# Kernel tuning notes

Measured on AMD Instinct MI355X. Metric: run time of the kernel, lower is better.

The kernel has to match this reference:

```python
import jax, jax.numpy as jnp
import numpy as np

DIM = 1024
HEADS = 16
HEAD_DIM = DIM // HEADS
SCALE = DIM ** -0.5  # note: original uses full dim, not head_dim


def setup_inputs() -> dict:
    key = jax.random.key(0)
    k1, k2, k3, k4 = jax.random.split(key, 4)
    x = jax.random.normal(k1, (4, 2048, DIM), dtype=jnp.float32)
    # nn.Linear(dim, 3*dim, bias=False): weight [3*dim, dim]; y = x @ W.T
    w_qkv = jax.random.normal(k2, (3 * DIM, DIM), dtype=jnp.float32) * (DIM ** -0.5)
    w_out = jax.random.normal(k3, (DIM, DIM), dtype=jnp.float32) * (DIM ** -0.5)
    b_out = jax.random.normal(k4, (DIM,), dtype=jnp.float32) * 0.01
    return {"x": x, "w_qkv": w_qkv, "w_out": w_out, "b_out": b_out}


def reference(x, w_qkv, w_out, b_out):
    b, n, d = x.shape
    qkv = jnp.einsum('bnd,ed->bne', x, w_qkv)  # [b, n, 3*dim]
    # rearrange 'b n (qkv h d) -> qkv b h n d'
    qkv = qkv.reshape(b, n, 3, HEADS, HEAD_DIM).transpose(2, 0, 3, 1, 4)
    q, k, v = qkv[0], qkv[1], qkv[2]
    dots = jnp.einsum('bhid,bhjd->bhij', q, k) * SCALE
    attn = jax.nn.softmax(dots, axis=-1)
    out = jnp.einsum('bhij,bhjd->bhid', attn, v)
    out = out.transpose(0, 2, 1, 3).reshape(b, n, d)  # b h n d -> b n (h d)
    return jnp.einsum('bnd,ed->bne', out, w_out) + b_out
```

## Files before the change

kernel.cpp:

```cpp
#include <hip/hip_runtime.h>
#include <stdint.h>
#include <stddef.h>

typedef _Float16 f16;
typedef __attribute__((ext_vector_type(8))) _Float16 f16x8;
typedef __attribute__((ext_vector_type(4))) _Float16 f16x4;
typedef __attribute__((ext_vector_type(4))) float f32x4;

#define DINL __device__ __forceinline__

DINL void async_cp16(void* lds, const void* gmem) {
    __builtin_amdgcn_global_load_lds(
        (const __attribute__((address_space(1))) void*)(uintptr_t)gmem,
        (__attribute__((address_space(3))) void*)(uint32_t)(uintptr_t)lds,
        16, 0, 0);
}

__global__ void cast_f32_f16(const float* __restrict__ src, f16* __restrict__ dst,
                             int n4, int scale_n4, float scale) {
    int stride = gridDim.x * blockDim.x;
    for (int i = blockIdx.x * blockDim.x + threadIdx.x; i < n4; i += stride) {
        float4 v = ((const float4*)src)[i];
        float s = (i < scale_n4) ? scale : 1.f;
        f16x4 h = { (f16)(v.x * s), (f16)(v.y * s), (f16)(v.z * s), (f16)(v.w * s) };
        ((f16x4*)dst)[i] = h;
    }
}

template <typename TC, bool HAS_BIAS>
__global__ __launch_bounds__(256) void gemm_bt(
    const f16* __restrict__ A, const f16* __restrict__ B,
    TC* __restrict__ C, const float* __restrict__ bias,
    int M, int N, int K)
{
    constexpr int BK = 64;
    __shared__ __align__(16) f16 As[128 * BK];
    __shared__ __align__(16) f16 Bs[128 * BK];

    const int tid  = threadIdx.x;
    const int lane = tid & 63;
    const int wave = tid >> 6;
    const int bm = blockIdx.y * 128;
    const int bn = blockIdx.x * 128;
    const int wr = (wave >> 1) * 64;
    const int wc = (wave & 1) * 64;

    f32x4 acc[4][4] = {};

    for (int k0 = 0; k0 < K; k0 += BK) {
#pragma unroll
        for (int it = 0; it < 4; ++it) {
            int s = tid + it * 256, row = s >> 3, cc = (s & 7) ^ (row & 7);
            async_cp16(&As[(size_t)s * 8], &A[(size_t)(bm + row) * K + k0 + cc * 8]);
        }
#pragma unroll
        for (int it = 0; it < 4; ++it) {
            int s = tid + it * 256, row = s >> 3, cc = (s & 7) ^ (row & 7);
            async_cp16(&Bs[(size_t)s * 8], &B[(size_t)(bn + row) * K + k0 + cc * 8]);
        }
        __syncthreads();

#pragma unroll
        for (int ks = 0; ks < BK; ks += 32) {
            const int rlo = lane & 15;
            const int c = (ks >> 3) + (lane >> 4);
            f16x8 af[4], bf[4];
#pragma unroll
            for (int m = 0; m < 4; ++m) {
                int r = wr + m * 16 + rlo;
                af[m] = *(const f16x8*)&As[(r * 8 + (c ^ (r & 7))) * 8];
            }
#pragma unroll
            for (int n = 0; n < 4; ++n) {
                int r = wc + n * 16 + rlo;
                bf[n] = *(const f16x8*)&Bs[(r * 8 + (c ^ (r & 7))) * 8];
            }
#pragma unroll
            for (int m = 0; m < 4; ++m)
#pragma unroll
                for (int n = 0; n < 4; ++n)
                    acc[m][n] = __builtin_amdgcn_mfma_f32_16x16x32_f16(af[m], bf[n], acc[m][n], 0, 0, 0);
        }
        __syncthreads();
    }

#pragma unroll
    for (int n = 0; n < 4; ++n) {
        const int gc = bn + wc + n * 16 + (lane & 15);
        float bv = 0.f;
        if constexpr (HAS_BIAS) bv = bias[gc];
#pragma unroll
        for (int m = 0; m < 4; ++m) {
            const int gr0 = bm + wr + m * 16 + ((lane >> 4) << 2);
#pragma unroll
            for (int r = 0; r < 4; ++r) {
                float v = acc[m][n][r] + bv;
                if constexpr (sizeof(TC) == 4) C[(size_t)(gr0 + r) * N + gc] = v;
                else                           C[(size_t)(gr0 + r) * N + gc] = (f16)v;
            }
        }
    }
}

__global__ __launch_bounds__(256) void transpose_v(const f16* __restrict__ qkv, f16* __restrict__ vt) {
    __shared__ float T[64][65];
    const int bid = blockIdx.x, bh = bid >> 5, st = bid & 31;
    const int b = bh >> 4, h = bh & 15, s0 = st * 64;
    const int tid = threadIdx.x;
    const int rs = tid >> 2, c0 = (tid & 3) * 16;
    const f16* src = &qkv[(size_t)(b * 2048 + s0 + rs) * 3072 + 2048 + h * 64 + c0];
    f16x8 v0 = ((const f16x8*)src)[0], v1 = ((const f16x8*)src)[1];
#pragma unroll
    for (int e = 0; e < 8; ++e) { T[rs][c0 + e] = (float)v0[e]; T[rs][c0 + 8 + e] = (float)v1[e]; }
    __syncthreads();
    const int rd = tid >> 2, k0 = (tid & 3) * 16;
    f16x8 w0, w1;
#pragma unroll
    for (int e = 0; e < 8; ++e) { w0[e] = (f16)T[k0 + e][rd]; w1[e] = (f16)T[k0 + 8 + e][rd]; }
    f16* dst = &vt[(size_t)(bh * 64 + rd) * 2048 + s0 + k0];
    ((f16x8*)dst)[0] = w0; ((f16x8*)dst)[1] = w1;
}

__global__ __launch_bounds__(256) void attn_mfma(
    const f16* __restrict__ qkv, const f16* __restrict__ vt, f16* __restrict__ out)
{
    constexpr int TD = 3072;
    __shared__ __align__(16) f16 Qs[128 * 64];
    __shared__ __align__(16) f16 Ks[64 * 64];
    __shared__ __align__(16) f16 Vs[64 * 64];
    __shared__ __align__(16) f16 Ps[4][32 * 64];

    const int tid = threadIdx.x, lane = tid & 63, wave = tid >> 6;
    const int bh = blockIdx.x, b = bh >> 4, h = bh & 15;
    const int q0 = blockIdx.y * 128;
    const size_t base = (size_t)b * 2048 * TD + h * 64;
    const int lo = lane & 15, hi = lane >> 4;

#pragma unroll
    for (int it = 0; it < 4; ++it) {
        int s = tid + it * 256, row = s >> 3, cc = (s & 7) ^ (row & 7);
        async_cp16(&Qs[s * 8], &qkv[base + (size_t)(q0 + row) * TD + cc * 8]);
    }

    float lp[2][4] = {};
    f32x4 o_[2][4] = {};

    for (int jt = 0; jt < 32; ++jt) {
        {
            int s = tid, row = s >> 3, cc = (s & 7) ^ (row & 7);
            int s2 = tid + 256, row2 = s2 >> 3, cc2 = (s2 & 7) ^ (row2 & 7);
            async_cp16(&Ks[s * 8],  &qkv[base + 1024 + (size_t)(jt * 64 + row)  * TD + cc * 8]);
            async_cp16(&Ks[s2 * 8], &qkv[base + 1024 + (size_t)(jt * 64 + row2) * TD + cc2 * 8]);
            async_cp16(&Vs[s * 8],  &vt[(size_t)(bh * 64 + row)  * 2048 + jt * 64 + cc * 8]);
            async_cp16(&Vs[s2 * 8], &vt[(size_t)(bh * 64 + row2) * 2048 + jt * 64 + cc2 * 8]);
        }
        __syncthreads();

        f32x4 sc[2][4] = {};
#pragma unroll
        for (int ks = 0; ks < 2; ++ks) {
            int c = ks * 4 + hi;
            f16x8 af[2];
#pragma unroll
            for (int m = 0; m < 2; ++m) {
                int r = wave * 32 + m * 16 + lo;
                af[m] = *(const f16x8*)&Qs[(r * 8 + (c ^ (r & 7))) * 8];
            }
#pragma unroll
            for (int n = 0; n < 4; ++n) {
                int key = n * 16 + lo;
                f16x8 bf = *(const f16x8*)&Ks[(key * 8 + (c ^ (key & 7))) * 8];
#pragma unroll
                for (int m = 0; m < 2; ++m)
                    sc[m][n] = __builtin_amdgcn_mfma_f32_16x16x32_f16(af[m], bf, sc[m][n], 0, 0, 0);
            }
        }

#pragma unroll
        for (int m = 0; m < 2; ++m) {
#pragma unroll
            for (int r = 0; r < 4; ++r) {
                float p0 = exp2f(sc[m][0][r]), p1 = exp2f(sc[m][1][r]);
                float p2 = exp2f(sc[m][2][r]), p3 = exp2f(sc[m][3][r]);
                lp[m][r] += (p0 + p1) + (p2 + p3);
                const int row_w = m * 16 + hi * 4 + r;
                const int rw7 = row_w & 7;
                const int ebase = row_w * 64 + (lo & 7);
                float pv[4] = { p0, p1, p2, p3 };
#pragma unroll
                for (int n = 0; n < 4; ++n) {
                    int chunk = n * 2 + (lo >> 3);
                    Ps[wave][ebase + ((chunk ^ rw7) << 3)] = (f16)pv[n];
                }
            }
        }
        asm volatile("s_waitcnt lgkmcnt(0)" ::: "memory");

#pragma unroll
        for (int ks = 0; ks < 2; ++ks) {
            int c = ks * 4 + hi;
            f16x8 pa[2];
#pragma unroll
            for (int m = 0; m < 2; ++m) {
                int r = m * 16 + lo;
                pa[m] = *(const f16x8*)&Ps[wave][(r * 8 + (c ^ (r & 7))) * 8];
            }
#pragma unroll
            for (int n = 0; n < 4; ++n) {
                int dd = n * 16 + lo;
                f16x8 vb = *(const f16x8*)&Vs[(dd * 8 + (c ^ (dd & 7))) * 8];
#pragma unroll
                for (int m = 0; m < 2; ++m)
                    o_[m][n] = __builtin_amdgcn_mfma_f32_16x16x32_f16(pa[m], vb, o_[m][n], 0, 0, 0);
            }
        }
        __syncthreads();
    }

#pragma unroll
    for (int m = 0; m < 2; ++m)
#pragma unroll
        for (int r = 0; r < 4; ++r) {
#pragma unroll
            for (int off = 1; off < 16; off <<= 1)
                lp[m][r] += __shfl_xor(lp[m][r], off);
            float inv = 1.f / lp[m][r];
            int row = q0 + wave * 32 + m * 16 + hi * 4 + r;
#pragma unroll
            for (int n = 0; n < 4; ++n) {
                int dim = h * 64 + n * 16 + lo;
                out[(size_t)(b * 2048 + row) * 1024 + dim] = (f16)(o_[m][n][r] * inv);
            }
        }
}

extern "C" void kernel_launch(void* const* d_in, const int* in_sizes, int n_in,
                              void* d_out, int out_size, void* d_ws, size_t ws_size,
                              hipStream_t stream)
{
    int ix = 0, iq = 1, iw = 2, ib = 3;
    for (int i = 0; i < n_in; ++i) {
        if      (in_sizes[i] == 8388608) ix = i;
        else if (in_sizes[i] == 3145728) iq = i;
        else if (in_sizes[i] == 1048576) iw = i;
        else if (in_sizes[i] == 1024)    ib = i;
    }
    const float* x     = (const float*)d_in[ix];
    const float* w_qkv = (const float*)d_in[iq];
    const float* w_out = (const float*)d_in[iw];
    const float* b_out = (const float*)d_in[ib];

    char* ws = (char*)d_ws;
    f16* Xh    = (f16*)(ws + 0);
    f16* AOh   = Xh;
    f16* Wqkvh = (f16*)(ws + 16777216);
    f16* Wouth = Wqkvh;
    f16* QKVh  = (f16*)(ws + 23068672);
    f16* Vth   = (f16*)(ws + 73400320);

    const float QSCALE = 0.03125f * 1.4426950408889634f;

    cast_f32_f16<<<2048, 256, 0, stream>>>(x,     Xh,    2097152, 0, 1.f);
    cast_f32_f16<<<1024, 256, 0, stream>>>(w_qkv, Wqkvh, 786432, 262144, QSCALE);

    gemm_bt<f16, false><<<dim3(24, 64), 256, 0, stream>>>(
        Xh, Wqkvh, QKVh, nullptr, 8192, 3072, 1024);

    cast_f32_f16<<<512, 256, 0, stream>>>(w_out, Wouth, 262144, 0, 1.f);

    transpose_v<<<2048, 256, 0, stream>>>(QKVh, Vth);

    attn_mfma<<<dim3(64, 16), 256, 0, stream>>>(QKVh, Vth, AOh);

    gemm_bt<float, true><<<dim3(8, 64), 256, 0, stream>>>(
        AOh, Wouth, (float*)d_out, b_out, 8192, 1024, 1024);
}
```

Before: 345.8 us.

## Double-buffer K/V tiles in attention, halve query tile, fuse cast kernels

The attention kernel now double-buffers K and V in LDS, prefetching the next tile while computing the current one, and drops one barrier per iteration. The query tile shrinks from 128 to 64 rows, so the grid doubles to 2048 blocks and each wave handles 16 rows instead of 32, which lowers register pressure and raises occupancy. The three f32-to-f16 cast launches are merged into one kernel, and w_out gets its own workspace slot so it no longer has to be cast after the QKV GEMM. In exchange, K/V are reloaded by twice as many blocks, and each K/V fragment read from LDS feeds half as many MFMAs.

```diff
diff --git a/kernel.cpp b/kernel.cpp
--- a/kernel.cpp
+++ b/kernel.cpp
@@ -16,14 +16,20 @@
         16, 0, 0);
 }
 
-__global__ void cast_f32_f16(const float* __restrict__ src, f16* __restrict__ dst,
-                             int n4, int scale_n4, float scale) {
+__global__ void cast_fused(const float* __restrict__ x, f16* __restrict__ xh,
+                           const float* __restrict__ wq, f16* __restrict__ wqh,
+                           const float* __restrict__ wo, f16* __restrict__ woh,
+                           float qs) {
     int stride = gridDim.x * blockDim.x;
-    for (int i = blockIdx.x * blockDim.x + threadIdx.x; i < n4; i += stride) {
-        float4 v = ((const float4*)src)[i];
-        float s = (i < scale_n4) ? scale : 1.f;
+    for (int i = blockIdx.x * blockDim.x + threadIdx.x; i < 3145728; i += stride) {
+        const float4* src; f16x4* dst; float s = 1.f;
+        if (i < 2097152)      { src = (const float4*)x  + i;            dst = (f16x4*)xh  + i; }
+        else if (i < 2883584) { int j = i - 2097152; src = (const float4*)wq + j; dst = (f16x4*)wqh + j;
+                                if (j < 262144) s = qs; }
+        else                  { int j = i - 2883584; src = (const float4*)wo + j; dst = (f16x4*)woh + j; }
+        float4 v = *src;
         f16x4 h = { (f16)(v.x * s), (f16)(v.y * s), (f16)(v.z * s), (f16)(v.w * s) };
-        ((f16x4*)dst)[i] = h;
+        *dst = h;
     }
 }
 
@@ -121,117 +127,105 @@
     ((f16x8*)dst)[0] = w0; ((f16x8*)dst)[1] = w1;
 }
 
+DINL void stage_kv(f16* Kd, f16* Vd, const f16* qkv, const f16* vt,
+                   size_t base, int bh, int jt, int tid) {
+    int s = tid, row = s >> 3, cc = (s & 7) ^ (row & 7);
+    int s2 = tid + 256, row2 = s2 >> 3, cc2 = (s2 & 7) ^ (row2 & 7);
+    async_cp16(&Kd[s * 8],  &qkv[base + 1024 + (size_t)(jt * 64 + row)  * 3072 + cc * 8]);
+    async_cp16(&Kd[s2 * 8], &qkv[base + 1024 + (size_t)(jt * 64 + row2) * 3072 + cc2 * 8]);
+    async_cp16(&Vd[s * 8],  &vt[(size_t)(bh * 64 + row)  * 2048 + jt * 64 + cc * 8]);
+    async_cp16(&Vd[s2 * 8], &vt[(size_t)(bh * 64 + row2) * 2048 + jt * 64 + cc2 * 8]);
+}
+
 __global__ __launch_bounds__(256) void attn_mfma(
     const f16* __restrict__ qkv, const f16* __restrict__ vt, f16* __restrict__ out)
 {
     constexpr int TD = 3072;
-    __shared__ __align__(16) f16 Qs[128 * 64];
-    __shared__ __align__(16) f16 Ks[64 * 64];
-    __shared__ __align__(16) f16 Vs[64 * 64];
-    __shared__ __align__(16) f16 Ps[4][32 * 64];
+    __shared__ __align__(16) f16 Qs[64 * 64];
+    __shared__ __align__(16) f16 Ks[2][64 * 64];
+    __shared__ __align__(16) f16 Vs[2][64 * 64];
+    __shared__ __align__(16) f16 Ps[4][16 * 64];
 
     const int tid = threadIdx.x, lane = tid & 63, wave = tid >> 6;
     const int bh = blockIdx.x, b = bh >> 4, h = bh & 15;
-    const int q0 = blockIdx.y * 128;
+    const int q0 = blockIdx.y * 64;
     const size_t base = (size_t)b * 2048 * TD + h * 64;
     const int lo = lane & 15, hi = lane >> 4;
 
 #pragma unroll
-    for (int it = 0; it < 4; ++it) {
+    for (int it = 0; it < 2; ++it) {
         int s = tid + it * 256, row = s >> 3, cc = (s & 7) ^ (row & 7);
         async_cp16(&Qs[s * 8], &qkv[base + (size_t)(q0 + row) * TD + cc * 8]);
     }
-
-    float lp[2][4] = {};
-    f32x4 o_[2][4] = {};
+    stage_kv(Ks[0], Vs[0], qkv, vt, base, bh, 0, tid);
+
+    float lp[4] = {};
+    f32x4 o_[4] = {};
 
     for (int jt = 0; jt < 32; ++jt) {
-        {
-            int s = tid, row = s >> 3, cc = (s & 7) ^ (row & 7);
-            int s2 = tid + 256, row2 = s2 >> 3, cc2 = (s2 & 7) ^ (row2 & 7);
-            async_cp16(&Ks[s * 8],  &qkv[base + 1024 + (size_t)(jt * 64 + row)  * TD + cc * 8]);
-            async_cp16(&Ks[s2 * 8], &qkv[base + 1024 + (size_t)(jt * 64 + row2) * TD + cc2 * 8]);
-            async_cp16(&Vs[s * 8],  &vt[(size_t)(bh * 64 + row)  * 2048 + jt * 64 + cc * 8]);
-            async_cp16(&Vs[s2 * 8], &vt[(size_t)(bh * 64 + row2) * 2048 + jt * 64 + cc2 * 8]);
-        }
+        const int cur = jt & 1;
         __syncthreads();
-
-        f32x4 sc[2][4] = {};
+        if (jt + 1 < 32)
+            stage_kv(Ks[cur ^ 1], Vs[cur ^ 1], qkv, vt, base, bh, jt + 1, tid);
+
+        f32x4 sc[4] = {};
 #pragma unroll
         for (int ks = 0; ks < 2; ++ks) {
-            int c = ks * 4 + hi;
-            f16x8 af[2];
-#pragma unroll
-            for (int m = 0; m < 2; ++m) {
-                int r = wave * 32 + m * 16 + lo;
-                af[m] = *(const f16x8*)&Qs[(r * 8 + (c ^ (r & 7))) * 8];
-            }
+            const int c = ks * 4 + hi;
+            const int r = wave * 16 + lo;
+            f16x8 af = *(const f16x8*)&Qs[(r * 8 + (c ^ (r & 7))) * 8];
 #pragma unroll
             for (int n = 0; n < 4; ++n) {
                 int key = n * 16 + lo;
-                f16x8 bf = *(const f16x8*)&Ks[(key * 8 + (c ^ (key & 7))) * 8];
-#pragma unroll
-                for (int m = 0; m < 2; ++m)
-                    sc[m][n] = __builtin_amdgcn_mfma_f32_16x16x32_f16(af[m], bf, sc[m][n], 0, 0, 0);
-            }
-        }
-
-#pragma unroll
-        for (int m = 0; m < 2; ++m) {
-#pragma unroll
-            for (int r = 0; r < 4; ++r) {
-                float p0 = exp2f(sc[m][0][r]), p1 = exp2f(sc[m][1][r]);
-                float p2 = exp2f(sc[m][2][r]), p3 = exp2f(sc[m][3][r]);
-                lp[m][r] += (p0 + p1) + (p2 + p3);
-                const int row_w = m * 16 + hi * 4 + r;
-                const int rw7 = row_w & 7;
-                const int ebase = row_w * 64 + (lo & 7);
-                float pv[4] = { p0, p1, p2, p3 };
-#pragma unroll
-                for (int n = 0; n < 4; ++n) {
-                    int chunk = n * 2 + (lo >> 3);
-                    Ps[wave][ebase + ((chunk ^ rw7) << 3)] = (f16)pv[n];
-                }
+                f16x8 bf = *(const f16x8*)&Ks[cur][(key * 8 + (c ^ (key & 7))) * 8];
+                sc[n] = __builtin_amdgcn_mfma_f32_16x16x32_f16(af, bf, sc[n], 0, 0, 0);
+            }
+        }
+
+#pragma unroll
+        for (int r = 0; r < 4; ++r) {
+            float p0 = exp2f(sc[0][r]), p1 = exp2f(sc[1][r]);
+            float p2 = exp2f(sc[2][r]), p3 = exp2f(sc[3][r]);
+            lp[r] += (p0 + p1) + (p2 + p3);
+            const int row_w = hi * 4 + r;
+            const int rw7 = row_w & 7;
+            const int ebase = row_w * 64 + (lo & 7);
+            float pv[4] = { p0, p1, p2, p3 };
+#pragma unroll
+            for (int n = 0; n < 4; ++n) {
+                int chunk = n * 2 + (lo >> 3);
+                Ps[wave][ebase + ((chunk ^ rw7) << 3)] = (f16)pv[n];
             }
         }
         asm volatile("s_waitcnt lgkmcnt(0)" ::: "memory");
 
 #pragma unroll
         for (int ks = 0; ks < 2; ++ks) {
-            int c = ks * 4 + hi;
-            f16x8 pa[2];
-#pragma unroll
-            for (int m = 0; m < 2; ++m) {
-                int r = m * 16 + lo;
-                pa[m] = *(const f16x8*)&Ps[wave][(r * 8 + (c ^ (r & 7))) * 8];
-            }
+            const int c = ks * 4 + hi;
+            const int r = lo;
+            f16x8 pa = *(const f16x8*)&Ps[wave][(r * 8 + (c ^ (r & 7))) * 8];
 #pragma unroll
             for (int n = 0; n < 4; ++n) {
                 int dd = n * 16 + lo;
-                f16x8 vb = *(const f16x8*)&Vs[(dd * 8 + (c ^ (dd & 7))) * 8];
-#pragma unroll
-                for (int m = 0; m < 2; ++m)
-                    o_[m][n] = __builtin_amdgcn_mfma_f32_16x16x32_f16(pa[m], vb, o_[m][n], 0, 0, 0);
-            }
-        }
-        __syncthreads();
-    }
-
-#pragma unroll
-    for (int m = 0; m < 2; ++m)
-#pragma unroll
-        for (int r = 0; r < 4; ++r) {
-#pragma unroll
-            for (int off = 1; off < 16; off <<= 1)
-                lp[m][r] += __shfl_xor(lp[m][r], off);
-            float inv = 1.f / lp[m][r];
-            int row = q0 + wave * 32 + m * 16 + hi * 4 + r;
-#pragma unroll
-            for (int n = 0; n < 4; ++n) {
-                int dim = h * 64 + n * 16 + lo;
-                out[(size_t)(b * 2048 + row) * 1024 + dim] = (f16)(o_[m][n][r] * inv);
-            }
-        }
+                f16x8 vb = *(const f16x8*)&Vs[cur][(dd * 8 + (c ^ (dd & 7))) * 8];
+                o_[n] = __builtin_amdgcn_mfma_f32_16x16x32_f16(pa, vb, o_[n], 0, 0, 0);
+            }
+        }
+    }
+
+#pragma unroll
+    for (int r = 0; r < 4; ++r) {
+#pragma unroll
+        for (int off = 1; off < 16; off <<= 1)
+            lp[r] += __shfl_xor(lp[r], off);
+        float inv = 1.f / lp[r];
+        int row = q0 + wave * 16 + hi * 4 + r;
+#pragma unroll
+        for (int n = 0; n < 4; ++n) {
+            int dim = h * 64 + n * 16 + lo;
+            out[(size_t)(b * 2048 + row) * 1024 + dim] = (f16)(o_[n][r] * inv);
+        }
+    }
 }
 
 extern "C" void kernel_launch(void* const* d_in, const int* in_sizes, int n_in,
@@ -254,23 +248,20 @@
     f16* Xh    = (f16*)(ws + 0);
     f16* AOh   = Xh;
     f16* Wqkvh = (f16*)(ws + 16777216);
-    f16* Wouth = Wqkvh;
     f16* QKVh  = (f16*)(ws + 23068672);
     f16* Vth   = (f16*)(ws + 73400320);
+    f16* Wouth = (f16*)(ws + 90177536);
 
     const float QSCALE = 0.03125f * 1.4426950408889634f;
 
-    cast_f32_f16<<<2048, 256, 0, stream>>>(x,     Xh,    2097152, 0, 1.f);
-    cast_f32_f16<<<1024, 256, 0, stream>>>(w_qkv, Wqkvh, 786432, 262144, QSCALE);
+    cast_fused<<<3072, 256, 0, stream>>>(x, Xh, w_qkv, Wqkvh, w_out, Wouth, QSCALE);
 
     gemm_bt<f16, false><<<dim3(24, 64), 256, 0, stream>>>(
         Xh, Wqkvh, QKVh, nullptr, 8192, 3072, 1024);
 
-    cast_f32_f16<<<512, 256, 0, stream>>>(w_out, Wouth, 262144, 0, 1.f);
-
     transpose_v<<<2048, 256, 0, stream>>>(QKVh, Vth);
 
-    attn_mfma<<<dim3(64, 16), 256, 0, stream>>>(QKVh, Vth, AOh);
+    attn_mfma<<<dim3(64, 32), 256, 0, stream>>>(QKVh, Vth, AOh);
 
     gemm_bt<float, true><<<dim3(8, 64), 256, 0, stream>>>(
         AOh, Wouth, (float*)d_out, b_out, 8192, 1024, 1024);
```

Measured after the change: 344.8 us. About the same (-0.3%).
